# Kernel optimization log

Measured on AMD Instinct MI355X. Metric: run time of the kernel, lower is better.

The kernel has to match this reference:

```python
import jax, jax.numpy as jnp
import numpy as np

DIM = 128
NH = 4
K = 7
PAD = K // 2  # dilation = 1
MLP_HID = 4 * DIM
EPS = 1e-5


def _layernorm(x, w, b):
    m = jnp.mean(x, axis=-1, keepdims=True)
    v = jnp.mean((x - m) ** 2, axis=-1, keepdims=True)
    return (x - m) / jnp.sqrt(v + EPS) * w + b


def _windows(xp, H, W):
    # xp: [B, nh, Hp, Wp, hd] zero-padded; returns [B, nh, H, W, hd, K*K]
    return jnp.stack(
        [xp[:, :, i:i + H, j:j + W, :] for i in range(K) for j in range(K)],
        axis=-1,
    )


def setup_inputs() -> dict:
    key = jax.random.key(0)
    ks = jax.random.split(key, 10)
    s = 0.02
    inp = {
        "x": jax.random.normal(ks[0], (4, 56, 56, DIM), dtype=jnp.float32),
        "ln1_w": jnp.ones((DIM,), jnp.float32),
        "ln1_b": jnp.zeros((DIM,), jnp.float32),
        "w_qkv": jax.random.normal(ks[1], (DIM, 3 * DIM), jnp.float32) * s,
        "b_qkv": jnp.zeros((3 * DIM,), jnp.float32),
        "rpb": jax.random.normal(ks[2], (NH, K * K), jnp.float32) * s,
        "w_proj": jax.random.normal(ks[3], (DIM, DIM), jnp.float32) * s,
        "b_proj": jnp.zeros((DIM,), jnp.float32),
        "ln2_w": jnp.ones((DIM,), jnp.float32),
        "ln2_b": jnp.zeros((DIM,), jnp.float32),
        "w_fc1": jax.random.normal(ks[4], (DIM, MLP_HID), jnp.float32) * s,
        "b_fc1": jnp.zeros((MLP_HID,), jnp.float32),
        "w_fc2": jax.random.normal(ks[5], (MLP_HID, DIM), jnp.float32) * s,
        "b_fc2": jnp.zeros((DIM,), jnp.float32),
    }
    return inp


def _nat_block(x, ln1_w, ln1_b, w_qkv, b_qkv, rpb, w_proj, b_proj,
               ln2_w, ln2_b, w_fc1, b_fc1, w_fc2, b_fc2):
    B, H, W, C = x.shape
    hd = C // NH
    scale = hd ** -0.5

    # --- neighborhood attention ---
    xn = _layernorm(x, ln1_w, ln1_b)
    qkv = xn @ w_qkv + b_qkv                       # [B,H,W,3C]
    qkv = qkv.reshape(B, H, W, 3, NH, hd)
    qkv = jnp.transpose(qkv, (3, 0, 4, 1, 2, 5))   # [3,B,nh,H,W,hd]
    q, k, v = qkv[0] * scale, qkv[1], qkv[2]
    # zero-pad spatial dims (matches F.pad with constant 0 in original)
    pad = ((0, 0), (0, 0), (PAD, PAD), (PAD, PAD), (0, 0))
    kp = jnp.pad(k, pad)
    vp = jnp.pad(v, pad)
    kw = _windows(kp, H, W)                        # [B,nh,H,W,hd,49]
    vw = _windows(vp, H, W)
    attn = jnp.einsum('bnhwd,bnhwdk->bnhwk', q, kw)
    attn = attn + rpb[None, :, None, None, :]
    attn = jax.nn.softmax(attn, axis=-1)
    out = jnp.einsum('bnhwk,bnhwdk->bnhwd', attn, vw)  # [B,nh,H,W,hd]
    out = jnp.transpose(out, (0, 2, 3, 1, 4)).reshape(B, H, W, C)
    x = x + (out @ w_proj + b_proj)

    # --- MLP ---
    xn2 = _layernorm(x, ln2_w, ln2_b)
    h = jax.nn.gelu(xn2 @ w_fc1 + b_fc1, approximate=False)
    x = x + (h @ w_fc2 + b_fc2)
    return x


def reference(x, ln1_w, ln1_b, w_qkv, b_qkv, rpb, w_proj, b_proj,
              ln2_w, ln2_b, w_fc1, b_fc1, w_fc2, b_fc2):
    return _nat_block(x, ln1_w, ln1_b, w_qkv, b_qkv, rpb, w_proj, b_proj,
                      ln2_w, ln2_b, w_fc1, b_fc1, w_fc2, b_fc2)
```

## Files before the change

kernel.cpp:

```cpp
#include <hip/hip_runtime.h>

using bf16x8 = __attribute__((ext_vector_type(8))) short;
using f32x4  = __attribute__((ext_vector_type(4))) float;
typedef unsigned short u16;
typedef __attribute__((ext_vector_type(8))) unsigned short u16x8;
typedef __attribute__((ext_vector_type(4))) unsigned short u16x4;

__device__ __forceinline__ u16 f2b(float f){
  unsigned int i=__float_as_uint(f);
  return (u16)((i + 0x7FFFu + ((i>>16)&1u))>>16);
}
__device__ __forceinline__ float b2f(u16 u){
  union{unsigned int i; float f;}v; v.i=((unsigned int)u)<<16; return v.f;
}
__device__ __forceinline__ void async16(const void* g, void* l){
  __builtin_amdgcn_global_load_lds((__attribute__((address_space(1))) void*)(g),
                                   (__attribute__((address_space(3))) void*)(l), 16, 0, 0);
}
__device__ __forceinline__ float gelu_tanh(float v){
  float u = v*(0.7978845608f + 0.0356774081f*v*v);
  float e = __expf(-2.0f*fabsf(u));
  float th = (1.0f-e)/(1.0f+e);
  th = (u<0.f)? -th : th;
  return 0.5f*v*(1.0f+th);
}

__global__ void prep_kernel(const float* __restrict__ wqkv, const float* __restrict__ wproj,
                            const float* __restrict__ wfc1, const float* __restrict__ wfc2,
                            u16* __restrict__ tqkv, u16* __restrict__ tproj,
                            u16* __restrict__ tfc1, u16* __restrict__ tfc2)
{
  int idx = blockIdx.x*256 + threadIdx.x;
  if (idx < 49152){
    int nc = idx>>14, r = idx&16383, i = r>>3, e = r&7, n = i&127, c = i>>7;
    tqkv[idx] = f2b(wqkv[(c*8+e)*384 + nc*128 + n]);
  } else if (idx < 65536){
    int r = idx-49152; int i=r>>3, e=r&7, n=i&127, c=i>>7;
    tproj[r] = f2b(wproj[(c*8+e)*128 + n]);
  } else if (idx < 131072){
    int t = idx-65536; int nc=t>>14, r=t&16383, i=r>>3, e=r&7, n=i&127, c=i>>7;
    tfc1[t] = f2b(wfc1[(c*8+e)*512 + nc*128 + n]);
  } else if (idx < 196608){
    int t = idx-131072; int nc=t>>14, r=t&16383, i=r>>3, e=r&7, n=i&127, c=i>>7;
    tfc2[t] = f2b(wfc2[(nc*128 + c*8 + e)*128 + n]);
  }
}


__global__ __launch_bounds__(256)
void qkv_ln_kernel(const float* __restrict__ x,
                   const float* __restrict__ ln1w, const float* __restrict__ ln1b,
                   const u16* __restrict__ tqkv, const float* __restrict__ bqkv,
                   u16* __restrict__ qb, u16* __restrict__ kb, u16* __restrict__ vb)
{
  __shared__ __align__(16) char smem[40960];
  char* lA = smem;
  char* lB = smem + 8192;

  const int tid = threadIdx.x;
  const int lane = tid&63, wid = tid>>6;
  const int quad = lane>>4, lrow = lane&15;
  const int m0 = blockIdx.x*32;
  const int nc = blockIdx.y;
  const int wm = (wid&1)*16, wn = (wid>>1)*64;

  #pragma unroll
  for (int kk=0;kk<8;kk++){
    int i = tid + kk*256;
    async16(tqkv + (size_t)nc*16384 + i*8, lB + i*16);
  }

  {
    const int row = tid>>3, g = tid&7;
    float xv[16];
    const float4* xr = (const float4*)(x + (size_t)(m0+row)*128 + g*16);
    float s=0.f, sq=0.f;
    #pragma unroll
    for (int c4=0;c4<4;c4++){
      float4 t = xr[c4];
      xv[c4*4]=t.x; xv[c4*4+1]=t.y; xv[c4*4+2]=t.z; xv[c4*4+3]=t.w;
      s += t.x+t.y+t.z+t.w;
      sq += t.x*t.x+t.y*t.y+t.z*t.z+t.w*t.w;
    }
    s  += __shfl_xor(s,1);  s  += __shfl_xor(s,2);  s  += __shfl_xor(s,4);
    sq += __shfl_xor(sq,1); sq += __shfl_xor(sq,2); sq += __shfl_xor(sq,4);
    float mean = s*0.0078125f;
    float rstd = rsqrtf(sq*0.0078125f - mean*mean + 1e-5f);
    const float4* wr = (const float4*)(ln1w + g*16);
    const float4* br = (const float4*)(ln1b + g*16);
    u16 nv[16];
    #pragma unroll
    for (int c4=0;c4<4;c4++){
      float4 w4 = wr[c4], b4 = br[c4];
      nv[c4*4]   = f2b((xv[c4*4]  -mean)*rstd*w4.x + b4.x);
      nv[c4*4+1] = f2b((xv[c4*4+1]-mean)*rstd*w4.y + b4.y);
      nv[c4*4+2] = f2b((xv[c4*4+2]-mean)*rstd*w4.z + b4.z);
      nv[c4*4+3] = f2b((xv[c4*4+3]-mean)*rstd*w4.w + b4.w);
    }
    #pragma unroll
    for (int cc=0;cc<2;cc++){
      u16x8 pk;
      #pragma unroll
      for (int e=0;e<8;e++) pk[e] = nv[cc*8+e];
      *(u16x8*)(lA + (((g*2+cc)*32 + row)<<4)) = pk;
    }
  }
  __syncthreads();

  f32x4 acc[4] = {};
  #pragma unroll
  for (int ks=0;ks<4;ks++){
    bf16x8 af = ((const bf16x8*)lA)[(ks*4+quad)*32 + wm + lrow];
    #pragma unroll
    for (int j=0;j<4;j++){
      bf16x8 bfr = ((const bf16x8*)lB)[(ks*4+quad)*128 + wn + j*16 + lrow];
      acc[j] = __builtin_amdgcn_mfma_f32_16x16x32_bf16(af, bfr, acc[j], 0,0,0);
    }
  }

  const float scale = 0.17677669529663687f;
  u16* dst = (nc==0)? qb : ((nc==1)? kb : vb);
  #pragma unroll
  for (int j=0;j<4;j++){
    int col = wn + j*16 + lrow;
    float bia = bqkv[nc*128 + col];
    #pragma unroll
    for (int r=0;r<4;r++){
      int row = m0 + wm + quad*4 + r;
      float val = acc[j][r] + bia;
      if (nc==0) val *= scale;
      dst[(size_t)row*128 + col] = f2b(val);
    }
  }
}

#define KT_S 40
#define VT_S 232
#define P_S  152
__global__ __launch_bounds__(256)
void attn_kernel(const u16* __restrict__ qb, const u16* __restrict__ kb,
                 const u16* __restrict__ vb, const float* __restrict__ rpb,
                 u16* __restrict__ aout)
{
  __shared__ __align__(16) char smem[50192];
  u16*  kt   = (u16*)smem;
  u16*  vt   = (u16*)(smem + 15680);
  u16*  Pm   = (u16*)(smem + 30528);
  float* srpb= (float*)(smem + 49984);

  const int tid = threadIdx.x;
  const int tile = blockIdx.x, bh = blockIdx.y;
  const int b = bh>>2, h = bh&3;
  const int ty = (tile/7)*8, tx = (tile%7)*8;
  const int lane = tid&63, wid = tid>>6;
  const int quad = lane>>4, lrow = lane&15;

  #pragma unroll
  for (int kk=0;kk<4;kk++){
    int i = tid + kk*256;
    if (i < 784){
      int pos = i>>2, oct = i&3;
      int hy = pos/14, hx = pos - hy*14;
      int gy = ty + hy - 3, gx = tx + hx - 3;
      u16x8 kv = {0,0,0,0,0,0,0,0};
      if (gy>=0 && gy<56 && gx>=0 && gx<56)
        kv = *(const u16x8*)(kb + ((size_t)(b*3136 + gy*56 + gx)*128 + h*32 + oct*8));
      *(u16x8*)(kt + pos*KT_S + oct*8) = kv;
    }
  }
  #pragma unroll
  for (int kk=0;kk<4;kk++){
    int i = tid + kk*256;
    if (i < 896){
      int pos = i>>2, oct = i&3;
      u16x8 vv = {0,0,0,0,0,0,0,0};
      if (pos < 196){
        int hy = pos/14, hx = pos - hy*14;
        int gy = ty + hy - 3, gx = tx + hx - 3;
        if (gy>=0 && gy<56 && gx>=0 && gx<56)
          vv = *(const u16x8*)(vb + ((size_t)(b*3136 + gy*56 + gx)*128 + h*32 + oct*8));
      }
      #pragma unroll
      for (int j=0;j<8;j++) vt[(oct*8+j)*VT_S + pos] = vv[j];
    }
  }
  if (tid < 49) srpb[tid] = rpb[h*49 + tid];
  __syncthreads();

  const int pxq = wid*16 + lrow;
  const int tokq = b*3136 + (ty + (pxq>>3))*56 + tx + (pxq&7);
  bf16x8 qf = *(const bf16x8*)(qb + (size_t)tokq*128 + h*32 + quad*8);

  f32x4 sc[7];
  const f32x4 zf = {0.f,0.f,0.f,0.f};
  #pragma unroll
  for (int cg=0;cg<7;cg++){
    int pos = wid*28 + cg*16 + lrow;
    bf16x8 kf = *(const bf16x8*)(kt + pos*KT_S + quad*8);
    sc[cg] = __builtin_amdgcn_mfma_f32_16x16x32_bf16(qf, kf, zf, 0,0,0);
  }

  const int lyq = quad>>1;
  #pragma unroll
  for (int cg=0;cg<7;cg++){
    int np = cg*16 + lrow;
    int nh = np/14, hx = np - nh*14;
    int dy = nh - lyq;
    #pragma unroll
    for (int r=0;r<4;r++){
      int lx = (quad*4+r)&7;
      int dx = hx - lx;
      bool in = ((unsigned)dy<7u) && ((unsigned)dx<7u);
      float bias = srpb[in ? (dy*7+dx) : 0];
      sc[cg][r] = in ? (sc[cg][r] + bias) : -1e30f;
    }
  }
  float inv[4];
  #pragma unroll
  for (int r=0;r<4;r++){
    float m = sc[0][r];
    #pragma unroll
    for (int cg=1;cg<7;cg++) m = fmaxf(m, sc[cg][r]);
    m = fmaxf(m, __shfl_xor(m,1)); m = fmaxf(m, __shfl_xor(m,2));
    m = fmaxf(m, __shfl_xor(m,4)); m = fmaxf(m, __shfl_xor(m,8));
    float l = 0.f;
    #pragma unroll
    for (int cg=0;cg<7;cg++){ float p = __expf(sc[cg][r]-m); sc[cg][r]=p; l+=p; }
    l += __shfl_xor(l,1); l += __shfl_xor(l,2);
    l += __shfl_xor(l,4); l += __shfl_xor(l,8);
    inv[r]=1.f/l;
  }

  u16* Pw = Pm + wid*16*P_S;
  #pragma unroll
  for (int cg=0;cg<7;cg++){
    int np = cg*16 + lrow;
    #pragma unroll
    for (int r=0;r<4;r++)
      Pw[(quad*4+r)*P_S + np] = f2b(sc[cg][r]);
  }
  { int zr = lane>>2, seg = lane&3;
    u16x4 z4 = {0,0,0,0};
    *(u16x4*)(Pw + zr*P_S + 112 + seg*4) = z4; }
  __syncthreads();

  f32x4 oacc[2] = {zf, zf};
  #pragma unroll
  for (int ks=0;ks<4;ks++){
    bf16x8 pf = *(const bf16x8*)(Pw + lrow*P_S + ks*32 + quad*8);
    #pragma unroll
    for (int cg2=0;cg2<2;cg2++){
      bf16x8 vf = *(const bf16x8*)(vt + (cg2*16+lrow)*VT_S + wid*28 + ks*32 + quad*8);
      oacc[cg2] = __builtin_amdgcn_mfma_f32_16x16x32_bf16(pf, vf, oacc[cg2], 0,0,0);
    }
  }
  #pragma unroll
  for (int r=0;r<4;r++){
    int px = wid*16 + quad*4 + r;
    int tok = b*3136 + (ty + (px>>3))*56 + tx + (px&7);
    #pragma unroll
    for (int cg2=0;cg2<2;cg2++){
      int ch = h*32 + cg2*16 + lrow;
      aout[(size_t)((tok>>5)*16 + (ch>>3))*256 + (tok&31)*8 + (ch&7)]
        = f2b(oacc[cg2][r]*inv[r]);
    }
  }
}

__global__ __launch_bounds__(256)
void mega_mlp_kernel(const u16* __restrict__ aout, const float* __restrict__ x,
                     const u16* __restrict__ tproj, const float* __restrict__ bproj,
                     const float* __restrict__ ln2w, const float* __restrict__ ln2b,
                     const u16* __restrict__ tfc1, const float* __restrict__ bfc1,
                     const u16* __restrict__ tfc2, const float* __restrict__ bfc2,
                     float* __restrict__ out)
{
  __shared__ __align__(16) char smem[49664];
  char* lA  = smem;
  char* lB  = smem + 8192;
  char* xn2 = smem + 40960;
  float* redS = (float*)(smem + 49152);
  float* redQ = redS + 64;

  const int tid = threadIdx.x;
  const int lane = tid&63, wid = tid>>6;
  const int quad = lane>>4, lrow = lane&15;
  const int m0 = blockIdx.x*32;
  const int wm = (wid&1)*16, wn = (wid>>1)*64;
  const int half = wid>>1;

  #pragma unroll
  for (int kk=0;kk<2;kk++){
    int i = tid + kk*256;
    async16(aout + (size_t)blockIdx.x*4096 + i*8, lA + i*16);
  }
  #pragma unroll
  for (int kk=0;kk<8;kk++){
    int i = tid + kk*256;
    async16(tproj + (size_t)i*8, lB + i*16);
  }
  __syncthreads();

  f32x4 acc[4] = {};
  #pragma unroll
  for (int ks=0;ks<4;ks++){
    bf16x8 af = ((const bf16x8*)lA)[(ks*4+quad)*32 + wm + lrow];
    #pragma unroll
    for (int j=0;j<4;j++){
      bf16x8 bfr = ((const bf16x8*)lB)[(ks*4+quad)*128 + wn + j*16 + lrow];
      acc[j] = __builtin_amdgcn_mfma_f32_16x16x32_bf16(af, bfr, acc[j], 0,0,0);
    }
  }

  float x1v[4][4];
  float ps[4] = {}, pq[4] = {};
  #pragma unroll
  for (int j=0;j<4;j++){
    int col = wn + j*16 + lrow;
    float bia = bproj[col];
    #pragma unroll
    for (int r=0;r<4;r++){
      int row = m0 + wm + quad*4 + r;
      float val = acc[j][r] + bia + x[(size_t)row*128 + col];
      x1v[j][r] = val;
      ps[r] += val; pq[r] += val*val;
    }
  }
  #pragma unroll
  for (int r=0;r<4;r++){
    #pragma unroll
    for (int off=1; off<16; off<<=1){
      ps[r] += __shfl_xor(ps[r], off);
      pq[r] += __shfl_xor(pq[r], off);
    }
  }
  if (lrow==0){
    #pragma unroll
    for (int r=0;r<4;r++){
      int row = wm + quad*4 + r;
      redS[half*32 + row] = ps[r];
      redQ[half*32 + row] = pq[r];
    }
  }
  __syncthreads();

  {
    float w2[4], b2[4];
    #pragma unroll
    for (int j=0;j<4;j++){ int col = wn+j*16+lrow; w2[j]=ln2w[col]; b2[j]=ln2b[col]; }
    #pragma unroll
    for (int r=0;r<4;r++){
      int row = wm + quad*4 + r;
      float mean = (redS[row] + redS[32+row])*0.0078125f;
      float var  = (redQ[row] + redQ[32+row])*0.0078125f - mean*mean;
      float rstd = rsqrtf(var + 1e-5f);
      #pragma unroll
      for (int j=0;j<4;j++){
        int col = wn + j*16 + lrow;
        u16 hv = f2b((x1v[j][r]-mean)*rstd*w2[j] + b2[j]);
        ((u16*)xn2)[((col>>3)*32 + row)*8 + (col&7)] = hv;
      }
    }
  }
  __syncthreads();

  f32x4 acc3[4] = {};
  for (int nc=0; nc<4; nc++){
    if (nc>0) __syncthreads();
    #pragma unroll
    for (int kk=0;kk<8;kk++){
      int i = tid + kk*256;
      async16(tfc1 + (size_t)nc*16384 + i*8, lB + i*16);
    }
    __syncthreads();

    f32x4 acc2[4] = {};
    #pragma unroll
    for (int ks=0;ks<4;ks++){
      bf16x8 af = ((const bf16x8*)xn2)[(ks*4+quad)*32 + wm + lrow];
      #pragma unroll
      for (int j=0;j<4;j++){
        bf16x8 bfr = ((const bf16x8*)lB)[(ks*4+quad)*128 + wn + j*16 + lrow];
        acc2[j] = __builtin_amdgcn_mfma_f32_16x16x32_bf16(af, bfr, acc2[j], 0,0,0);
      }
    }
    #pragma unroll
    for (int j=0;j<4;j++){
      int col = wn + j*16 + lrow;
      float bia = bfc1[nc*128 + col];
      #pragma unroll
      for (int r=0;r<4;r++){
        int row = wm + quad*4 + r;
        float g = gelu_tanh(acc2[j][r] + bia);
        ((u16*)lA)[((col>>3)*32 + row)*8 + (col&7)] = f2b(g);
      }
    }
    __syncthreads();
    #pragma unroll
    for (int kk=0;kk<8;kk++){
      int i = tid + kk*256;
      async16(tfc2 + (size_t)nc*16384 + i*8, lB + i*16);
    }
    __syncthreads();

    #pragma unroll
    for (int ks=0;ks<4;ks++){
      bf16x8 af = ((const bf16x8*)lA)[(ks*4+quad)*32 + wm + lrow];
      #pragma unroll
      for (int j=0;j<4;j++){
        bf16x8 bfr = ((const bf16x8*)lB)[(ks*4+quad)*128 + wn + j*16 + lrow];
        acc3[j] = __builtin_amdgcn_mfma_f32_16x16x32_bf16(af, bfr, acc3[j], 0,0,0);
      }
    }
  }

  #pragma unroll
  for (int j=0;j<4;j++){
    int col = wn + j*16 + lrow;
    float bia = bfc2[col];
    #pragma unroll
    for (int r=0;r<4;r++){
      int row = m0 + wm + quad*4 + r;
      out[(size_t)row*128 + col] = acc3[j][r] + bia + x1v[j][r];
    }
  }
}

extern "C" void kernel_launch(void* const* d_in, const int* in_sizes, int n_in,
                              void* d_out, int out_size, void* d_ws, size_t ws_size,
                              hipStream_t stream)
{
  const float* x     =(const float*)d_in[0];
  const float* ln1w  =(const float*)d_in[1];
  const float* ln1b  =(const float*)d_in[2];
  const float* wqkv  =(const float*)d_in[3];
  const float* bqkv  =(const float*)d_in[4];
  const float* rpb   =(const float*)d_in[5];
  const float* wproj =(const float*)d_in[6];
  const float* bproj =(const float*)d_in[7];
  const float* ln2w  =(const float*)d_in[8];
  const float* ln2b  =(const float*)d_in[9];
  const float* wfc1  =(const float*)d_in[10];
  const float* bfc1  =(const float*)d_in[11];
  const float* wfc2  =(const float*)d_in[12];
  const float* bfc2  =(const float*)d_in[13];

  char* ws=(char*)d_ws;
  size_t o=0;
  u16* tqkv =(u16*)(ws+o); o+=98304;
  u16* tproj=(u16*)(ws+o); o+=32768;
  u16* tfc1 =(u16*)(ws+o); o+=131072;
  u16* tfc2 =(u16*)(ws+o); o+=131072;
  u16* aout =(u16*)(ws+o); o+=3211264;
  u16* qb   =(u16*)(ws+o); o+=3211264;
  u16* kb   =(u16*)(ws+o); o+=3211264;
  u16* vb   =(u16*)(ws+o); o+=3211264;

  prep_kernel<<<768,256,0,stream>>>(wqkv,wproj,wfc1,wfc2,tqkv,tproj,tfc1,tfc2);
  qkv_ln_kernel<<<dim3(392,3),256,0,stream>>>(x,ln1w,ln1b,tqkv,bqkv,qb,kb,vb);
  attn_kernel<<<dim3(49,16),256,0,stream>>>(qb,kb,vb,rpb,aout);
  mega_mlp_kernel<<<392,256,0,stream>>>(aout,x,tproj,bproj,ln2w,ln2b,
                                        tfc1,bfc1,tfc2,bfc2,(float*)d_out);
}
```

Baseline: 129.1 us.

## Triple-buffer MLP weight staging with explicit waitcnt pipeline and 64-row tiles

Rewrites the fused proj+LN2+MLP kernel to use 512 threads and 64-row tiles, halving the grid to 196 blocks, with three 32KB LDS weight buffers. Weight chunks for fc1/fc2 are prefetched asynchronously ahead of use, using manual vmcnt/lgkmcnt waits and raw barriers instead of __syncthreads, and MFMA sections run at raised wave priority. This is meant to hide weight-load latency and amortize each weight load over twice as many rows. In exchange it uses 128KB of LDS per block (one block per CU) and leaves only 196 blocks, which underfills the 256 CUs. The hand-counted waitcnt values also risk races if the count of in-flight loads per thread is wrong.

After: 128.3 us. About the same (-0.6%).

```diff
diff --git a/kernel.cpp b/kernel.cpp
--- a/kernel.cpp
+++ b/kernel.cpp
@@ -24,6 +24,12 @@
   th = (u<0.f)? -th : th;
   return 0.5f*v*(1.0f+th);
 }
+
+#define BARX() do{ __asm__ volatile("" ::: "memory"); \
+                   __builtin_amdgcn_s_barrier(); \
+                   __asm__ volatile("" ::: "memory"); }while(0)
+#define WAITV(n) __asm__ volatile("s_waitcnt vmcnt(" #n ")" ::: "memory")
+#define WAITL()  __asm__ volatile("s_waitcnt lgkmcnt(0)" ::: "memory")
 
 __global__ void prep_kernel(const float* __restrict__ wqkv, const float* __restrict__ wproj,
                             const float* __restrict__ wfc1, const float* __restrict__ wfc2,
@@ -267,7 +273,47 @@
   }
 }
 
-__global__ __launch_bounds__(256)
+
+__device__ __forceinline__ void stage32k(const u16* __restrict__ src, char* dst, int tid){
+  #pragma unroll
+  for (int kk=0;kk<4;kk++){ int i = tid + kk*512; async16(src + (size_t)i*8, dst + i*16); }
+}
+
+__device__ __forceinline__ void mfma16(const char* Ab, const char* Bb,
+                                       int quad, int lrow, int wm, int wn, f32x4 acc[4]){
+  const int row = wm + lrow;
+  #pragma unroll
+  for (int ks=0;ks<4;ks++){
+    bf16x8 af = ((const bf16x8*)Ab)[(row>>5)*512 + (ks*4+quad)*32 + (row&31)];
+    #pragma unroll
+    for (int j=0;j<4;j++){
+      bf16x8 bfr = ((const bf16x8*)Bb)[(ks*4+quad)*128 + wn + j*16 + lrow];
+      acc[j] = __builtin_amdgcn_mfma_f32_16x16x32_bf16(af, bfr, acc[j], 0,0,0);
+    }
+  }
+}
+
+__device__ __forceinline__ void fc1_phase(const char* xn2, const char* B, char* lA,
+                                          const float* __restrict__ bfc1c,
+                                          int quad, int lrow, int wm, int wn){
+  f32x4 a2[4] = {};
+  __builtin_amdgcn_s_setprio(1);
+  mfma16(xn2, B, quad, lrow, wm, wn, a2);
+  __builtin_amdgcn_s_setprio(0);
+  #pragma unroll
+  for (int j=0;j<4;j++){
+    int col = wn + j*16 + lrow;
+    float bia = bfc1c[col];
+    #pragma unroll
+    for (int r=0;r<4;r++){
+      int row = wm + quad*4 + r;
+      float g = gelu_tanh(a2[j][r] + bia);
+      ((u16*)lA)[(row>>5)*4096 + ((col>>3)*32 + (row&31))*8 + (col&7)] = f2b(g);
+    }
+  }
+}
+
+__global__ __launch_bounds__(512)
 void mega_mlp_kernel(const u16* __restrict__ aout, const float* __restrict__ x,
                      const u16* __restrict__ tproj, const float* __restrict__ bproj,
                      const float* __restrict__ ln2w, const float* __restrict__ ln2b,
@@ -275,144 +321,134 @@
                      const u16* __restrict__ tfc2, const float* __restrict__ bfc2,
                      float* __restrict__ out)
 {
-  __shared__ __align__(16) char smem[49664];
-  char* lA  = smem;
-  char* lB  = smem + 8192;
-  char* xn2 = smem + 40960;
-  float* redS = (float*)(smem + 49152);
-  float* redQ = redS + 64;
+  __shared__ __align__(16) char smem[131072];
+  char* B0  = smem;
+  char* B1  = smem + 32768;
+  char* B2  = smem + 65536;
+  char* lA  = smem + 98304;
+  char* xn2 = smem + 114688;
+  float* redS = (float*)lA;
+  float* redQ = redS + 128;
 
   const int tid = threadIdx.x;
   const int lane = tid&63, wid = tid>>6;
   const int quad = lane>>4, lrow = lane&15;
-  const int m0 = blockIdx.x*32;
-  const int wm = (wid&1)*16, wn = (wid>>1)*64;
-  const int half = wid>>1;
-
+  const int m0 = blockIdx.x*64;
+  const int wm = (wid&3)*16, wn = (wid>>2)*64;
+  const int half = wid>>2;
+
+  float xv[4][4];
+  #pragma unroll
+  for (int j=0;j<4;j++){
+    #pragma unroll
+    for (int r=0;r<4;r++)
+      xv[j][r] = x[(size_t)(m0+wm+quad*4+r)*128 + wn + j*16 + lrow];
+  }
+
+  stage32k(tproj, B0, tid);
   #pragma unroll
   for (int kk=0;kk<2;kk++){
-    int i = tid + kk*256;
-    async16(aout + (size_t)blockIdx.x*4096 + i*8, lA + i*16);
-  }
-  #pragma unroll
-  for (int kk=0;kk<8;kk++){
-    int i = tid + kk*256;
-    async16(tproj + (size_t)i*8, lB + i*16);
-  }
-  __syncthreads();
+    int i = tid + kk*512;
+    async16(aout + (size_t)blockIdx.x*8192 + i*8, lA + i*16);
+  }
+  stage32k(tfc1,           B1, tid);
+  stage32k(tfc2,           B2, tid);
+  WAITV(8); BARX();
 
   f32x4 acc[4] = {};
-  #pragma unroll
-  for (int ks=0;ks<4;ks++){
-    bf16x8 af = ((const bf16x8*)lA)[(ks*4+quad)*32 + wm + lrow];
-    #pragma unroll
-    for (int j=0;j<4;j++){
-      bf16x8 bfr = ((const bf16x8*)lB)[(ks*4+quad)*128 + wn + j*16 + lrow];
-      acc[j] = __builtin_amdgcn_mfma_f32_16x16x32_bf16(af, bfr, acc[j], 0,0,0);
-    }
-  }
-
-  float x1v[4][4];
-  float ps[4] = {}, pq[4] = {};
+  __builtin_amdgcn_s_setprio(1);
+  mfma16(lA, B0, quad, lrow, wm, wn, acc);
+  __builtin_amdgcn_s_setprio(0);
+  float x1v[4][4]; float ps[4]={0,0,0,0}, pq[4]={0,0,0,0};
   #pragma unroll
   for (int j=0;j<4;j++){
-    int col = wn + j*16 + lrow;
-    float bia = bproj[col];
-    #pragma unroll
-    for (int r=0;r<4;r++){
-      int row = m0 + wm + quad*4 + r;
-      float val = acc[j][r] + bia + x[(size_t)row*128 + col];
-      x1v[j][r] = val;
-      ps[r] += val; pq[r] += val*val;
+    float bia = bproj[wn + j*16 + lrow];
+    #pragma unroll
+    for (int r=0;r<4;r++){
+      float val = acc[j][r] + bia + xv[j][r];
+      x1v[j][r] = val; ps[r]+=val; pq[r]+=val*val;
     }
   }
   #pragma unroll
   for (int r=0;r<4;r++){
     #pragma unroll
     for (int off=1; off<16; off<<=1){
-      ps[r] += __shfl_xor(ps[r], off);
-      pq[r] += __shfl_xor(pq[r], off);
-    }
-  }
+      ps[r]+=__shfl_xor(ps[r],off); pq[r]+=__shfl_xor(pq[r],off);
+    }
+  }
+  BARX();
+  stage32k(tfc1 + 16384,   B0, tid);
   if (lrow==0){
     #pragma unroll
     for (int r=0;r<4;r++){
       int row = wm + quad*4 + r;
-      redS[half*32 + row] = ps[r];
-      redQ[half*32 + row] = pq[r];
-    }
-  }
-  __syncthreads();
+      redS[half*64+row]=ps[r]; redQ[half*64+row]=pq[r];
+    }
+  }
+  WAITL(); WAITV(8); BARX();
 
   {
     float w2[4], b2[4];
     #pragma unroll
-    for (int j=0;j<4;j++){ int col = wn+j*16+lrow; w2[j]=ln2w[col]; b2[j]=ln2b[col]; }
+    for (int j=0;j<4;j++){ int col=wn+j*16+lrow; w2[j]=ln2w[col]; b2[j]=ln2b[col]; }
     #pragma unroll
     for (int r=0;r<4;r++){
       int row = wm + quad*4 + r;
-      float mean = (redS[row] + redS[32+row])*0.0078125f;
-      float var  = (redQ[row] + redQ[32+row])*0.0078125f - mean*mean;
+      float mean = (redS[row]+redS[64+row])*0.0078125f;
+      float var  = (redQ[row]+redQ[64+row])*0.0078125f - mean*mean;
       float rstd = rsqrtf(var + 1e-5f);
       #pragma unroll
       for (int j=0;j<4;j++){
         int col = wn + j*16 + lrow;
-        u16 hv = f2b((x1v[j][r]-mean)*rstd*w2[j] + b2[j]);
-        ((u16*)xn2)[((col>>3)*32 + row)*8 + (col&7)] = hv;
+        ((u16*)xn2)[(row>>5)*4096 + ((col>>3)*32 + (row&31))*8 + (col&7)]
+          = f2b((x1v[j][r]-mean)*rstd*w2[j] + b2[j]);
       }
     }
   }
-  __syncthreads();
+  WAITL(); BARX();
 
   f32x4 acc3[4] = {};
-  for (int nc=0; nc<4; nc++){
-    if (nc>0) __syncthreads();
-    #pragma unroll
-    for (int kk=0;kk<8;kk++){
-      int i = tid + kk*256;
-      async16(tfc1 + (size_t)nc*16384 + i*8, lB + i*16);
-    }
-    __syncthreads();
-
-    f32x4 acc2[4] = {};
-    #pragma unroll
-    for (int ks=0;ks<4;ks++){
-      bf16x8 af = ((const bf16x8*)xn2)[(ks*4+quad)*32 + wm + lrow];
-      #pragma unroll
-      for (int j=0;j<4;j++){
-        bf16x8 bfr = ((const bf16x8*)lB)[(ks*4+quad)*128 + wn + j*16 + lrow];
-        acc2[j] = __builtin_amdgcn_mfma_f32_16x16x32_bf16(af, bfr, acc2[j], 0,0,0);
-      }
-    }
-    #pragma unroll
-    for (int j=0;j<4;j++){
-      int col = wn + j*16 + lrow;
-      float bia = bfc1[nc*128 + col];
-      #pragma unroll
-      for (int r=0;r<4;r++){
-        int row = wm + quad*4 + r;
-        float g = gelu_tanh(acc2[j][r] + bia);
-        ((u16*)lA)[((col>>3)*32 + row)*8 + (col&7)] = f2b(g);
-      }
-    }
-    __syncthreads();
-    #pragma unroll
-    for (int kk=0;kk<8;kk++){
-      int i = tid + kk*256;
-      async16(tfc2 + (size_t)nc*16384 + i*8, lB + i*16);
-    }
-    __syncthreads();
-
-    #pragma unroll
-    for (int ks=0;ks<4;ks++){
-      bf16x8 af = ((const bf16x8*)lA)[(ks*4+quad)*32 + wm + lrow];
-      #pragma unroll
-      for (int j=0;j<4;j++){
-        bf16x8 bfr = ((const bf16x8*)lB)[(ks*4+quad)*128 + wn + j*16 + lrow];
-        acc3[j] = __builtin_amdgcn_mfma_f32_16x16x32_bf16(af, bfr, acc3[j], 0,0,0);
-      }
-    }
-  }
+
+  fc1_phase(xn2, B1, lA, bfc1, quad, lrow, wm, wn);
+  WAITL(); BARX();
+  stage32k(tfc2 + 16384,   B1, tid);
+  WAITV(8); BARX();
+
+  __builtin_amdgcn_s_setprio(1);
+  mfma16(lA, B2, quad, lrow, wm, wn, acc3);
+  __builtin_amdgcn_s_setprio(0);
+  BARX();
+  stage32k(tfc1 + 2*16384, B2, tid);
+  WAITV(8); BARX();
+
+  fc1_phase(xn2, B0, lA, bfc1 + 128, quad, lrow, wm, wn);
+  WAITL(); BARX();
+  stage32k(tfc2 + 2*16384, B0, tid);
+  WAITV(8); BARX();
+
+  __builtin_amdgcn_s_setprio(1);
+  mfma16(lA, B1, quad, lrow, wm, wn, acc3);
+  __builtin_amdgcn_s_setprio(0);
+  BARX();
+  stage32k(tfc1 + 3*16384, B1, tid);
+  WAITV(8); BARX();
+
+  fc1_phase(xn2, B2, lA, bfc1 + 256, quad, lrow, wm, wn);
+  WAITL(); BARX();
+  stage32k(tfc2 + 3*16384, B2, tid);
+  WAITV(8); BARX();
+
+  __builtin_amdgcn_s_setprio(1);
+  mfma16(lA, B0, quad, lrow, wm, wn, acc3);
+  __builtin_amdgcn_s_setprio(0);
+  WAITV(4); BARX();
+
+  fc1_phase(xn2, B1, lA, bfc1 + 384, quad, lrow, wm, wn);
+  WAITL(); WAITV(0); BARX();
+
+  __builtin_amdgcn_s_setprio(1);
+  mfma16(lA, B2, quad, lrow, wm, wn, acc3);
+  __builtin_amdgcn_s_setprio(0);
 
   #pragma unroll
   for (int j=0;j<4;j++){
@@ -459,6 +495,6 @@
   prep_kernel<<<768,256,0,stream>>>(wqkv,wproj,wfc1,wfc2,tqkv,tproj,tfc1,tfc2);
   qkv_ln_kernel<<<dim3(392,3),256,0,stream>>>(x,ln1w,ln1b,tqkv,bqkv,qb,kb,vb);
   attn_kernel<<<dim3(49,16),256,0,stream>>>(qb,kb,vb,rpb,aout);
-  mega_mlp_kernel<<<392,256,0,stream>>>(aout,x,tproj,bproj,ln2w,ln2b,
+  mega_mlp_kernel<<<196,512,0,stream>>>(aout,x,tproj,bproj,ln2w,ln2b,
                                         tfc1,bfc1,tfc2,bfc2,(float*)d_out);
 }
```
